# Kernel optimization log

Hardware: AMD Instinct MI355X
Metric: run time of the kernel (lower is better)

The kernel has to match this reference:

```python
import jax, jax.numpy as jnp
import numpy as np

# Production-scale dims: b=8, t=1024, emb=1024, heads=16 -> head dim s=64.
B, T, E, H = 8, 1024, 1024, 16
S = E // H  # 64, per-head dim; tokeys/toqueries/tovalues are Linear(S, S) shared across heads


def setup_inputs() -> dict:
    key = jax.random.key(0)
    k0, k1, k2, k3, k4, k5 = jax.random.split(key, 6)
    return {
        "x": jax.random.normal(k0, (B, T, E), dtype=jnp.float32),
        # full lengths: keeps the length-mask path live without all--inf rows (NaN softmax)
        "lengths": jnp.full((B,), T, dtype=jnp.int32),
        # torch Linear stores weight as (out_features, in_features); y = x @ W.T
        "Wk": jax.random.normal(k1, (S, S), dtype=jnp.float32) / np.float32(np.sqrt(S)),
        "Wq": jax.random.normal(k2, (S, S), dtype=jnp.float32) / np.float32(np.sqrt(S)),
        "Wv": jax.random.normal(k3, (S, S), dtype=jnp.float32) / np.float32(np.sqrt(S)),
        "Wu": jax.random.normal(k4, (E, E), dtype=jnp.float32) / np.float32(np.sqrt(E)),
        "bu": jax.random.normal(k5, (E,), dtype=jnp.float32) * jnp.float32(0.02),
    }


def reference(x, lengths, Wk, Wq, Wv, Wu, bu):
    b, t, e = x.shape
    h = H
    s = e // h
    xh = x.reshape(b, t, h, s)

    # per-head projections (same S x S weight for every head), torch Linear: x @ W.T
    queries = jnp.einsum('bths,os->btho', xh, Wq)
    keys = jnp.einsum('bths,os->btho', xh, Wk)
    values = jnp.einsum('bths,os->btho', xh, Wv)

    # scale q and k each by e**-0.25 (net 1/sqrt(e) on scores)
    scale = jnp.float32(e) ** jnp.float32(-0.25)
    dot = jnp.einsum('bqho,bkho->bhqk', queries * scale, keys * scale)  # (b,h,t,t)

    # causal mask (mask_diagonal=False -> strictly upper triangle masked)
    i = jnp.arange(t)[:, None]
    j = jnp.arange(t)[None, :]
    causal = j <= i  # (t,t)
    # length mask over key positions: key index k < lengths[b]
    lenmask = jnp.arange(t)[None, :] < lengths[:, None]  # (b,t)
    valid = causal[None, None, :, :] & lenmask[:, None, None, :]  # (b,1->h,t,t)

    dot = jnp.where(valid, dot, -jnp.inf)
    attn = jax.nn.softmax(dot, axis=-1)

    out = jnp.einsum('bhqk,bkho->bqho', attn, values).reshape(b, t, e)
    return jnp.einsum('bte,oe->bto', out, Wu) + bu
```

## Files before the change

kernel.cpp:

```cpp
#include <hip/hip_runtime.h>
#include <stdint.h>

#define B_ 8
#define T_ 1024
#define E_ 1024
#define H_ 16
#define S_ 64

typedef __attribute__((ext_vector_type(8))) short bf16x8;
typedef __attribute__((ext_vector_type(4))) short bf16x4;
typedef __attribute__((ext_vector_type(4))) float f32x4;

__device__ __forceinline__ f32x4 mfma_pv(bf16x4 a, bf16x4 b, f32x4 c) {
  return __builtin_amdgcn_mfma_f32_16x16x16bf16_1k(a, b, c, 0, 0, 0);
}

__device__ __forceinline__ float e2(float x) { return __builtin_amdgcn_exp2f(x); }

__device__ __forceinline__ ushort f2bf(float f) {
  union { float f; uint32_t u; } v; v.f = f;
  uint32_t r = (v.u + 0x7FFFu + ((v.u >> 16) & 1u)) >> 16;
  return (ushort)r;
}
__device__ __forceinline__ float bf2f(ushort u) {
  union { uint32_t u; float f; } v; v.u = ((uint32_t)u) << 16;
  return v.f;
}

__device__ __forceinline__ uint32_t pk2(float a, float b) {
  return __builtin_amdgcn_perm(__float_as_uint(b) + 0x8000u,
                               __float_as_uint(a) + 0x8000u, 0x07060302u);
}
__device__ __forceinline__ bf16x4 pack4(const float* p) {
  union { uint32_t u[2]; bf16x4 v; } pu;
  pu.u[0] = pk2(p[0], p[1]);
  pu.u[1] = pk2(p[2], p[3]);
  return pu.v;
}

__device__ __forceinline__ void gload_lds16(const ushort* g, ushort* l) {
  __builtin_amdgcn_global_load_lds(
      (const __attribute__((address_space(1))) uint32_t*)g,
      (__attribute__((address_space(3))) uint32_t*)l, 16, 0, 0);
}

__device__ __forceinline__ bf16x8 load8(const void* p, size_t idx, bool isf32) {
  if (isf32) {
    const float* fp = (const float*)p + idx;
    f32x4 f0 = *(const f32x4*)(fp);
    f32x4 f1 = *(const f32x4*)(fp + 4);
    bf16x8 r;
    #pragma unroll
    for (int i = 0; i < 4; ++i) r[i] = (short)f2bf(f0[i]);
    #pragma unroll
    for (int i = 0; i < 4; ++i) r[4 + i] = (short)f2bf(f1[i]);
    return r;
  }
  return *(const bf16x8*)((const ushort*)p + idx);
}

__device__ __forceinline__ bool detect_f32_wave(const uint32_t* __restrict__ x) {
  const int lane = threadIdx.x & 63;
  int sane = 0;
  #pragma unroll
  for (int j = 0; j < 4; ++j) {
    uint32_t lo = x[lane * 4 + j] & 0xFFFFu;
    uint32_t e = (lo >> 7) & 0xFFu;
    sane += (e >= 96u && e <= 158u) ? 1 : 0;
  }
  #pragma unroll
  for (int off = 32; off >= 1; off >>= 1) sane += __shfl_xor(sane, off);
  return sane < 192;
}

__global__ __launch_bounds__(256) void cvt_kernel(
    const void* __restrict__ x,
    const void* __restrict__ Wu, const void* __restrict__ bu,
    const void* __restrict__ Wq, const void* __restrict__ Wk,
    const void* __restrict__ Wv,
    ushort* __restrict__ wub, ushort* __restrict__ bub,
    ushort* __restrict__ wqkv) {
  const bool f32 = detect_f32_wave((const uint32_t*)x);
  if (blockIdx.x < 512) {
    size_t base = (size_t)blockIdx.x * 2048 + threadIdx.x * 8;
    *(bf16x8*)(wub + base) = load8(Wu, base, f32);
  } else if (blockIdx.x == 512) {
    if (threadIdx.x < 128) {
      size_t base = (size_t)threadIdx.x * 8;
      *(bf16x8*)(bub + base) = load8(bu, base, f32);
    }
  } else {
    const void* Ws[3] = {Wq, Wk, Wv};
    int idx = blockIdx.x - 513;
    int w = idx >> 1, half = idx & 1;
    size_t base = (size_t)half * 2048 + threadIdx.x * 8;
    *(bf16x8*)(wqkv + w * 4096 + base) = load8(Ws[w], base, f32);
  }
}

#define QSCALE 0.045084220f

__global__ __launch_bounds__(256) void qkv_kernel(
    const void* __restrict__ x, const ushort* __restrict__ wqkv,
    ushort* __restrict__ qb, ushort* __restrict__ kb, ushort* __restrict__ vb) {
  __shared__ ushort qs[64 * 72];
  __shared__ ushort ks[64 * 72];
  __shared__ ushort vs[64 * 72];
  const bool f32 = detect_f32_wave((const uint32_t*)x);
  const int tid = threadIdx.x;
  const int lane = tid & 63, wave = tid >> 6;
  const int m = lane & 15, quad = lane >> 4;
  const int tile = blockIdx.x & 15;
  const int h = (blockIdx.x >> 4) & 15;
  const int b = blockIdx.x >> 8;
  const int t0 = tile * 64;

  const size_t xrow = ((size_t)b * T_ + t0 + wave * 16 + m) * E_ + h * S_;
  bf16x8 a0 = load8(x, xrow + quad * 8, f32);
  bf16x8 a1 = load8(x, xrow + 32 + quad * 8, f32);

  #pragma unroll
  for (int w = 0; w < 3; ++w) {
    const float sc = (w == 0) ? QSCALE : 1.0f;
    ushort* dst = (w == 0) ? qs : (w == 1) ? ks : vs;
    #pragma unroll
    for (int nt = 0; nt < 4; ++nt) {
      const ushort* wrow = wqkv + w * 4096 + (nt * 16 + m) * S_;
      bf16x8 b0 = *(const bf16x8*)(wrow + quad * 8);
      bf16x8 b1 = *(const bf16x8*)(wrow + 32 + quad * 8);
      f32x4 acc = {0.f, 0.f, 0.f, 0.f};
      acc = __builtin_amdgcn_mfma_f32_16x16x32_bf16(a0, b0, acc, 0, 0, 0);
      acc = __builtin_amdgcn_mfma_f32_16x16x32_bf16(a1, b1, acc, 0, 0, 0);
      #pragma unroll
      for (int i = 0; i < 4; ++i) {
        int lr = wave * 16 + quad * 4 + i;
        int o  = nt * 16 + m;
        if (w == 2) {
          vs[o * 72 + lr] = f2bf(acc[i]);
        } else {
          dst[lr * 72 + o] = f2bf(acc[i] * sc);
        }
      }
    }
  }

  __syncthreads();

  const int row = tid >> 2, ck = (tid & 3) * 16;
  const size_t qkbase = (((size_t)b * H_ + h) * T_ + t0 + row) * S_ + ck;
  *(bf16x8*)(qb + qkbase)     = *(const bf16x8*)(qs + row * 72 + ck);
  *(bf16x8*)(qb + qkbase + 8) = *(const bf16x8*)(qs + row * 72 + ck + 8);
  *(bf16x8*)(kb + qkbase)     = *(const bf16x8*)(ks + row * 72 + ck);
  *(bf16x8*)(kb + qkbase + 8) = *(const bf16x8*)(ks + row * 72 + ck + 8);
  const size_t vbase = (((size_t)b * H_ + h) * S_ + row) * T_ + t0 + ck;
  *(bf16x8*)(vb + vbase)      = *(const bf16x8*)(vs + row * 72 + ck);
  *(bf16x8*)(vb + vbase + 8)  = *(const bf16x8*)(vs + row * 72 + ck + 8);
}

__global__ __launch_bounds__(256, 3) void attn_kernel(
    const ushort* __restrict__ qb, const ushort* __restrict__ kb,
    const ushort* __restrict__ vb, const int* __restrict__ lengths,
    ushort* __restrict__ ao) {
  __shared__ ushort klds[2][64 * 64];
  __shared__ ushort vlds[2][64 * 64];

  const int tid = threadIdx.x;
  const int lane = tid & 63, wave = tid >> 6;
  const int m = lane & 15, quad = lane >> 4;
  const int ord = blockIdx.x >> 7;
  const int bh = blockIdx.x & 127;
  const int b  = bh >> 4, h = bh & 15;
  const int qt = 15 - ord;
  const int len = lengths[b];

  const size_t head_off = ((size_t)b * H_ + h) * (size_t)T_ * S_;
  const ushort* Q  = qb + head_off;
  const ushort* K  = kb + head_off;
  const ushort* Vt = vb + head_off;

  const int sr  = lane >> 3;
  const int ssw = 8 * ((lane & 7) ^ sr);
  const int swzr = 8 * (m & 7);

  const int qw = qt * 64 + wave * 16;
  bf16x8 aq0 = *(const bf16x8*)(Q + (size_t)(qw + m) * S_ + quad * 8);
  bf16x8 aq1 = *(const bf16x8*)(Q + (size_t)(qw + m) * S_ + 32 + quad * 8);

  const int qmin = min(qw + m, len - 1);

  f32x4 o[4], Lacc;
  #pragma unroll
  for (int i = 0; i < 4; ++i) o[i] = (f32x4){0.f, 0.f, 0.f, 0.f};
  Lacc = (f32x4){0.f, 0.f, 0.f, 0.f};

  bf16x4 ones;
  #pragma unroll
  for (int i = 0; i < 4; ++i) ones[i] = (short)0x3F80;

  #pragma unroll
  for (int p = 0; p < 2; ++p) {
    const int wrow = wave * 16 + p * 8;
    gload_lds16(K  + (size_t)(wrow + sr) * S_ + ssw, &klds[0][wrow * 64]);
    gload_lds16(Vt + (size_t)(wrow + sr) * T_ + ssw, &vlds[0][wrow * 64]);
  }
  __syncthreads();

  for (int kt = 0; kt <= qt; ++kt) {
    const bool msk = (kt == qt) || ((kt + 1) * 64 > len);

    if (kt < qt) {
      const ushort* Kn = K + (size_t)(kt + 1) * 64 * S_;
      #pragma unroll
      for (int p = 0; p < 2; ++p) {
        const int wrow = wave * 16 + p * 8;
        gload_lds16(Kn + (size_t)(wrow + sr) * S_ + ssw,
                    &klds[(kt + 1) & 1][wrow * 64]);
        gload_lds16(Vt + (size_t)(wrow + sr) * T_ + (kt + 1) * 64 + ssw,
                    &vlds[(kt + 1) & 1][wrow * 64]);
      }
    }

    const ushort* kls = klds[kt & 1];
    const ushort* vls = vlds[kt & 1];

    bf16x4 vv[4][4];
    #pragma unroll
    for (int nt = 0; nt < 4; ++nt) {
      #pragma unroll
      for (int v4 = 0; v4 < 4; ++v4) {
        vv[nt][v4] = *(const bf16x4*)(vls + (v4 * 16 + m) * 64 +
                                      8 * ((2 * nt + (quad >> 1)) ^ (m & 7)) +
                                      (quad & 1) * 4);
      }
    }

    bf16x4 pf[4];
    #pragma unroll
    for (int nt = 0; nt < 4; ++nt) {
      const ushort* krow = kls + (nt * 16 + m) * 64;
      bf16x8 ak0 = *(const bf16x8*)(krow + ((8 * quad) ^ swzr));
      bf16x8 ak1 = *(const bf16x8*)(krow + ((32 + 8 * quad) ^ swzr));
      const int kl0 = kt * 64 + nt * 16 + quad * 4;

      __builtin_amdgcn_s_setprio(1);
      f32x4 s4 = {0.f, 0.f, 0.f, 0.f};
      s4 = __builtin_amdgcn_mfma_f32_16x16x32_bf16(ak0, aq0, s4, 0, 0, 0);
      s4 = __builtin_amdgcn_mfma_f32_16x16x32_bf16(ak1, aq1, s4, 0, 0, 0);
      __builtin_amdgcn_s_setprio(0);

      float p4[4];
      #pragma unroll
      for (int i = 0; i < 4; ++i) {
        float s = s4[i];
        if (msk) s = (kl0 + i <= qmin) ? s : -1e30f;
        p4[i] = e2(s);
      }
      pf[nt] = pack4(p4);
    }

    __builtin_amdgcn_s_setprio(1);
    #pragma unroll
    for (int nt = 0; nt < 4; ++nt) {
      Lacc = mfma_pv(pf[nt], ones, Lacc);
      #pragma unroll
      for (int v4 = 0; v4 < 4; ++v4)
        o[v4] = mfma_pv(pf[nt], vv[nt][v4], o[v4]);
    }
    __builtin_amdgcn_s_setprio(0);

    if (kt < qt) __syncthreads();
  }

  #pragma unroll
  for (int i = 0; i < 4; ++i) {
    float il = (Lacc[i] > 0.f) ? 1.0f / Lacc[i] : 0.f;
    size_t base = ((size_t)b * T_ + qw + quad * 4 + i) * E_ + h * 64;
    #pragma unroll
    for (int v4 = 0; v4 < 4; ++v4)
      ao[base + v4 * 16 + m] = f2bf(o[v4][i] * il);
  }
}

__global__ __launch_bounds__(256) void proj_kernel(
    const ushort* __restrict__ A, const ushort* __restrict__ Wu,
    const ushort* __restrict__ bu, float* __restrict__ Y) {
  __shared__ ushort As[128 * 72];
  __shared__ ushort Bs[128 * 72];
  const int tid = threadIdx.x;
  const int lane = tid & 63, wave = tid >> 6;
  const int m = lane & 15, quad = lane >> 4;
  const int m0 = blockIdx.x * 128, n0 = blockIdx.y * 128;
  const int wm = (wave & 1) * 64, wn = (wave >> 1) * 64;

  f32x4 acc[4][4];
  #pragma unroll
  for (int i = 0; i < 4; ++i)
    #pragma unroll
    for (int j = 0; j < 4; ++j) acc[i][j] = (f32x4){0.f, 0.f, 0.f, 0.f};

  bf16x8 pa[4], pb[4];
  #pragma unroll
  for (int p = 0; p < 4; ++p) {
    int c = tid + p * 256;
    int row = c >> 3, col = (c & 7) * 8;
    pa[p] = *(const bf16x8*)(A + (size_t)(m0 + row) * E_ + col);
    pb[p] = *(const bf16x8*)(Wu + (size_t)(n0 + row) * E_ + col);
  }

  for (int k0 = 0; k0 < E_; k0 += 64) {
    __syncthreads();
    #pragma unroll
    for (int p = 0; p < 4; ++p) {
      int c = tid + p * 256;
      int row = c >> 3, col = (c & 7) * 8;
      *(bf16x8*)(As + row * 72 + col) = pa[p];
      *(bf16x8*)(Bs + row * 72 + col) = pb[p];
    }
    __syncthreads();

    if (k0 + 64 < E_) {
      #pragma unroll
      for (int p = 0; p < 4; ++p) {
        int c = tid + p * 256;
        int row = c >> 3, col = (c & 7) * 8;
        pa[p] = *(const bf16x8*)(A + (size_t)(m0 + row) * E_ + k0 + 64 + col);
        pb[p] = *(const bf16x8*)(Wu + (size_t)(n0 + row) * E_ + k0 + 64 + col);
      }
    }

    #pragma unroll
    for (int kk = 0; kk < 64; kk += 32) {
      bf16x8 af[4], bfrag[4];
      #pragma unroll
      for (int i = 0; i < 4; ++i)
        af[i] = *(const bf16x8*)(As + (wm + i * 16 + m) * 72 + kk + quad * 8);
      #pragma unroll
      for (int j = 0; j < 4; ++j)
        bfrag[j] = *(const bf16x8*)(Bs + (wn + j * 16 + m) * 72 + kk + quad * 8);
      #pragma unroll
      for (int i = 0; i < 4; ++i)
        #pragma unroll
        for (int j = 0; j < 4; ++j)
          acc[i][j] = __builtin_amdgcn_mfma_f32_16x16x32_bf16(af[i], bfrag[j], acc[i][j], 0, 0, 0);
    }
  }

  #pragma unroll
  for (int j = 0; j < 4; ++j) {
    float bias = bf2f(bu[n0 + wn + j * 16 + m]);
    #pragma unroll
    for (int i = 0; i < 4; ++i) {
      #pragma unroll
      for (int r = 0; r < 4; ++r) {
        int grow = m0 + wm + i * 16 + quad * 4 + r;
        int gcol = n0 + wn + j * 16 + m;
        Y[(size_t)grow * E_ + gcol] = acc[i][j][r] + bias;
      }
    }
  }
}

extern "C" void kernel_launch(void* const* d_in, const int* in_sizes, int n_in,
                              void* d_out, int out_size, void* d_ws, size_t ws_size,
                              hipStream_t stream) {
  const void* x  = d_in[0];
  const int* lengths = (const int*)d_in[1];
  const void* Wk = d_in[2];
  const void* Wq = d_in[3];
  const void* Wv = d_in[4];
  const void* Wu = d_in[5];
  const void* bu = d_in[6];
  float* out = (float*)d_out;

  const size_t hsz = (size_t)B_ * H_ * T_ * S_;
  ushort* qb   = (ushort*)d_ws;
  ushort* kb   = qb + hsz;
  ushort* vb   = kb + hsz;
  ushort* ao   = vb + hsz;
  ushort* wub  = ao + hsz;
  ushort* bub  = wub + (size_t)E_ * E_;
  ushort* wqkv = bub + E_;

  cvt_kernel<<<dim3(519), dim3(256), 0, stream>>>(x, Wu, bu, Wq, Wk, Wv, wub, bub, wqkv);
  qkv_kernel<<<dim3(B_ * H_ * (T_ / 64)), dim3(256), 0, stream>>>(x, wqkv, qb, kb, vb);
  attn_kernel<<<dim3(B_ * H_ * 16), dim3(256), 0, stream>>>(qb, kb, vb, lengths, ao);
  proj_kernel<<<dim3((B_ * T_) / 128, E_ / 128), dim3(256), 0, stream>>>(ao, wub, bub, out);
}
```

Before: 183.1 us.

## Use direct global-to-LDS loads with XOR swizzle and XCD-aware tiling in projection

Swaps the manual f32-to-bf16 rounding and the perm-based packing for the hardware v_cvt_pk_bf16_f32 instruction. The output projection GEMM now copies tiles straight from global memory into LDS with global_load_lds, replacing the register-staged prefetch. To avoid bank conflicts without row padding, the LDS tiles use an XOR swizzle. The 1D grid is remapped so that blocks on the same XCD share rows of A for better L2 reuse. Dropping the register prefetch means global latency is no longer overlapped with compute inside a block, and the rounding behaviour of the packing conversion may differ slightly.

```diff
diff --git a/kernel.cpp b/kernel.cpp
--- a/kernel.cpp
+++ b/kernel.cpp
@@ -27,14 +27,15 @@
   return v.f;
 }
 
-__device__ __forceinline__ uint32_t pk2(float a, float b) {
-  return __builtin_amdgcn_perm(__float_as_uint(b) + 0x8000u,
-                               __float_as_uint(a) + 0x8000u, 0x07060302u);
+__device__ __forceinline__ uint32_t cvtpk(float a, float b) {
+  uint32_t r;
+  asm("v_cvt_pk_bf16_f32 %0, %1, %2" : "=v"(r) : "v"(a), "v"(b));
+  return r;
 }
 __device__ __forceinline__ bf16x4 pack4(const float* p) {
   union { uint32_t u[2]; bf16x4 v; } pu;
-  pu.u[0] = pk2(p[0], p[1]);
-  pu.u[1] = pk2(p[2], p[3]);
+  pu.u[0] = cvtpk(p[0], p[1]);
+  pu.u[1] = cvtpk(p[2], p[3]);
   return pu.v;
 }
 
@@ -49,12 +50,12 @@
     const float* fp = (const float*)p + idx;
     f32x4 f0 = *(const f32x4*)(fp);
     f32x4 f1 = *(const f32x4*)(fp + 4);
-    bf16x8 r;
-    #pragma unroll
-    for (int i = 0; i < 4; ++i) r[i] = (short)f2bf(f0[i]);
-    #pragma unroll
-    for (int i = 0; i < 4; ++i) r[4 + i] = (short)f2bf(f1[i]);
-    return r;
+    union { uint32_t u[4]; bf16x8 v; } r;
+    r.u[0] = cvtpk(f0[0], f0[1]);
+    r.u[1] = cvtpk(f0[2], f0[3]);
+    r.u[2] = cvtpk(f1[0], f1[1]);
+    r.u[3] = cvtpk(f1[2], f1[3]);
+    return r.v;
   }
   return *(const bf16x8*)((const ushort*)p + idx);
 }
@@ -284,59 +285,49 @@
 __global__ __launch_bounds__(256) void proj_kernel(
     const ushort* __restrict__ A, const ushort* __restrict__ Wu,
     const ushort* __restrict__ bu, float* __restrict__ Y) {
-  __shared__ ushort As[128 * 72];
-  __shared__ ushort Bs[128 * 72];
+  __shared__ ushort As[128 * 64];
+  __shared__ ushort Bs[128 * 64];
   const int tid = threadIdx.x;
   const int lane = tid & 63, wave = tid >> 6;
   const int m = lane & 15, quad = lane >> 4;
-  const int m0 = blockIdx.x * 128, n0 = blockIdx.y * 128;
+
+  const int orig = blockIdx.x;
+  const int xcd = orig & 7, slot = orig >> 3;
+  const int m0 = (xcd * 8 + (slot >> 3)) * 128;
+  const int n0 = (slot & 7) * 128;
   const int wm = (wave & 1) * 64, wn = (wave >> 1) * 64;
 
+  const int sr  = lane >> 3;
+  const int ssw = 8 * ((lane & 7) ^ sr);
+  const int swzr = 8 * (m & 7);
+
   f32x4 acc[4][4];
   #pragma unroll
   for (int i = 0; i < 4; ++i)
     #pragma unroll
     for (int j = 0; j < 4; ++j) acc[i][j] = (f32x4){0.f, 0.f, 0.f, 0.f};
-
-  bf16x8 pa[4], pb[4];
-  #pragma unroll
-  for (int p = 0; p < 4; ++p) {
-    int c = tid + p * 256;
-    int row = c >> 3, col = (c & 7) * 8;
-    pa[p] = *(const bf16x8*)(A + (size_t)(m0 + row) * E_ + col);
-    pb[p] = *(const bf16x8*)(Wu + (size_t)(n0 + row) * E_ + col);
-  }
 
   for (int k0 = 0; k0 < E_; k0 += 64) {
     __syncthreads();
     #pragma unroll
     for (int p = 0; p < 4; ++p) {
-      int c = tid + p * 256;
-      int row = c >> 3, col = (c & 7) * 8;
-      *(bf16x8*)(As + row * 72 + col) = pa[p];
-      *(bf16x8*)(Bs + row * 72 + col) = pb[p];
+      const int wrow = wave * 32 + p * 8;
+      gload_lds16(A  + (size_t)(m0 + wrow + sr) * E_ + k0 + ssw, As + wrow * 64);
+      gload_lds16(Wu + (size_t)(n0 + wrow + sr) * E_ + k0 + ssw, Bs + wrow * 64);
     }
     __syncthreads();
-
-    if (k0 + 64 < E_) {
-      #pragma unroll
-      for (int p = 0; p < 4; ++p) {
-        int c = tid + p * 256;
-        int row = c >> 3, col = (c & 7) * 8;
-        pa[p] = *(const bf16x8*)(A + (size_t)(m0 + row) * E_ + k0 + 64 + col);
-        pb[p] = *(const bf16x8*)(Wu + (size_t)(n0 + row) * E_ + k0 + 64 + col);
-      }
-    }
 
     #pragma unroll
     for (int kk = 0; kk < 64; kk += 32) {
       bf16x8 af[4], bfrag[4];
       #pragma unroll
       for (int i = 0; i < 4; ++i)
-        af[i] = *(const bf16x8*)(As + (wm + i * 16 + m) * 72 + kk + quad * 8);
+        af[i] = *(const bf16x8*)(As + (wm + i * 16 + m) * 64 +
+                                 ((kk + 8 * quad) ^ swzr));
       #pragma unroll
       for (int j = 0; j < 4; ++j)
-        bfrag[j] = *(const bf16x8*)(Bs + (wn + j * 16 + m) * 72 + kk + quad * 8);
+        bfrag[j] = *(const bf16x8*)(Bs + (wn + j * 16 + m) * 64 +
+                                    ((kk + 8 * quad) ^ swzr));
       #pragma unroll
       for (int i = 0; i < 4; ++i)
         #pragma unroll
@@ -384,5 +375,5 @@
   cvt_kernel<<<dim3(519), dim3(256), 0, stream>>>(x, Wu, bu, Wq, Wk, Wv, wub, bub, wqkv);
   qkv_kernel<<<dim3(B_ * H_ * (T_ / 64)), dim3(256), 0, stream>>>(x, wqkv, qb, kb, vb);
   attn_kernel<<<dim3(B_ * H_ * 16), dim3(256), 0, stream>>>(qb, kb, vb, lengths, ao);
-  proj_kernel<<<dim3((B_ * T_) / 128, E_ / 128), dim3(256), 0, stream>>>(ao, wub, bub, out);
-}
+  proj_kernel<<<dim3(512), dim3(256), 0, stream>>>(ao, wub, bub, out);
+}
```

After: 184.2 us. No clear change (+0.6%).
